# Kernel optimization log

Hardware: AMD Instinct MI355X
Metric: run time of the kernel (lower is better)

The kernel has to match this reference:

```python
import jax, jax.numpy as jnp
import numpy as np

EPS = 1e-12  # torch F.normalize eps


def _normalize(x):
    n = jnp.sqrt(jnp.sum(x * x, axis=1, keepdims=True))
    return x / jnp.maximum(n, EPS)


def _exp_sim(a, b, temp):
    # exp(a @ b.T / temp); returns (diag [B], row_sum [B,1])
    m = jnp.exp(jnp.matmul(a, b.T) / temp)
    return jnp.diagonal(m), jnp.sum(m, axis=1, keepdims=True)


def reference(x):
    temp = 0.1
    bsz = x.shape[0] // 3
    xn = _normalize(x)
    xe, ye, ze = xn[:bsz], xn[bsz:2 * bsz], xn[2 * bsz:]

    d_xx, s_xx = _exp_sim(xe, xe, temp)
    d_yy, s_yy = _exp_sim(ye, ye, temp)
    d_xy, s_xy = _exp_sim(xe, ye, temp)
    d_ax, s_ax = _exp_sim(xe, ze, temp)
    d_ay, s_ay = _exp_sim(ye, ze, temp)
    d_zx, s_zx = _exp_sim(ze, xe, temp)
    d_zy, s_zy = _exp_sim(ze, ye, temp)

    # NOTE: diag terms are [B], row-sums are [B,1] -> denominator broadcasts to
    # [B,B], matching the original torch broadcasting exactly.
    denom_mutual = (s_xy - d_xy) + (s_xx - d_xx) + (s_yy - d_yy)  # [B,B]
    loss_mutual = jnp.mean(-2.0 * jnp.log(d_xy / denom_mutual))

    def aux(d, s):
        return jnp.mean(-jnp.log(d / (s - d)))  # d/[B,B] -> [B,B]

    loss = (loss_mutual + aux(d_ax, s_ax) + aux(d_ay, s_ay)
            + aux(d_zx, s_zx) + aux(d_zy, s_zy))
    return loss


def setup_inputs() -> dict:
    key = jax.random.key(0)
    x = jax.random.normal(key, (12288, 128), dtype=jnp.float32)
    return {"x": x}
```

## Files before the change

### kernel.cpp

```cpp
#include <hip/hip_runtime.h>
#include <hip/hip_bf16.h>


typedef __attribute__((ext_vector_type(8))) short short8;
typedef __attribute__((ext_vector_type(4))) float floatx4;

#define D   128
#define BSZ 4096
#define GPM 256
#define GRID_EXPSIM (5 * 16 * 16)

__global__ __launch_bounds__(256) void normalize_kernel(
    const float* __restrict__ x, __hip_bfloat162* __restrict__ xnf2,
    float* __restrict__ out, int rows) {
  int tid = threadIdx.x;
  if (blockIdx.x == 0 && tid == 0) out[0] = 0.0f;

  int row  = blockIdx.x * 4 + (tid >> 6);
  int lane = tid & 63;
  if (row >= rows) return;
  const float2* xr = (const float2*)(x + (size_t)row * D);
  float2 v = xr[lane];
  float s = v.x * v.x + v.y * v.y;
#pragma unroll
  for (int off = 1; off < 64; off <<= 1) s += __shfl_xor(s, off, 64);
  float scale = 3.7982825470322528f / fmaxf(sqrtf(s), 1e-12f);
  __hip_bfloat162 h;
  h.x = __float2bfloat16(v.x * scale);
  h.y = __float2bfloat16(v.y * scale);
  int g    = row >> 4;
  int kk   = lane >> 4;
  int quad = (lane >> 2) & 3;
  int jj   = lane & 3;
  xnf2[g * 1024 + kk * 256 + (quad * 16 + (row & 15)) * 4 + jj] = h;
}

template <bool COL, bool DIAG>
__device__ __forceinline__ void epilogue(
    const floatx4 (&acc)[4][4], float (&rs)[4][4], float (&cs)[4],
    int rowg0, int colg0, int quad, int lm, float* __restrict__ diag_ptr) {
#pragma unroll
  for (int mi = 0; mi < 4; mi++) {
#pragma unroll
    for (int r = 0; r < 4; r++) {
      int rowg = rowg0 + mi * 16 + quad * 4 + r;
      float part = 0.f;
#pragma unroll
      for (int ni = 0; ni < 4; ni++) {
        float e = __builtin_amdgcn_exp2f(acc[mi][ni][r]);
        part += e;
        if (COL) cs[ni] += e;
        if (DIAG) {
          if (colg0 + ni * 16 + lm == rowg) diag_ptr[rowg] = e;
        }
      }
      rs[mi][r] += part;
    }
  }
}

__global__ __launch_bounds__(256) void expsim_kernel(
    const short8* __restrict__ xnf8,
    float* __restrict__ srow,
    float* __restrict__ scol,
    float* __restrict__ diag) {
  __shared__ float csLDS[4 * 256];

  int tid = threadIdx.x;
  int bx  = blockIdx.x;
  int task = bx >> 8;
  int rem  = bx & 255;
  int rb   = rem >> 4;
  int cb   = rem & 15;

  const int aoff_t[5] = {0, 1, 0, 0, 1};
  const int boff_t[5] = {0, 1, 1, 2, 2};
  bool col_en = (task >= 3);

  int w    = tid >> 6;
  int lane = tid & 63;
  int quad = lane >> 4;
  int lm   = lane & 15;
  int rowg0 = rb * 256 + w * 64;

  bool dgblk = (rb == cb);

  float* diag_ptr = diag + task * BSZ;

  int gA = aoff_t[task] * GPM + rb * 16 + w * 4;
  short8 afrag[4][4];
#pragma unroll
  for (int mi = 0; mi < 4; mi++)
#pragma unroll
    for (int kk = 0; kk < 4; kk++)
      afrag[mi][kk] = xnf8[(size_t)(gA + mi) * 256 + kk * 64 + lane];

  float rs[4][4];
#pragma unroll
  for (int mi = 0; mi < 4; mi++)
#pragma unroll
    for (int r = 0; r < 4; r++) rs[mi][r] = 0.0f;

  const floatx4 z4 = {0.f, 0.f, 0.f, 0.f};
  const short8* bbase = xnf8 + (size_t)(boff_t[task] * GPM + cb * 16) * 256 + lane;

#pragma unroll 1
  for (int t = 0; t < 4; t++) {
    int colg0 = cb * 256 + t * 64;

    short8 bf[16];
#pragma unroll
    for (int i = 0; i < 16; i++)
      bf[i] = bbase[(size_t)(t * 4 + (i & 3)) * 256 + (i >> 2) * 64];

    floatx4 acc[4][4];
#pragma unroll
    for (int kk = 0; kk < 4; kk++)
#pragma unroll
      for (int mi = 0; mi < 4; mi++)
#pragma unroll
        for (int ni = 0; ni < 4; ni++)
          acc[mi][ni] = __builtin_amdgcn_mfma_f32_16x16x32_bf16(
              afrag[mi][kk], bf[kk * 4 + ni], (kk == 0) ? z4 : acc[mi][ni],
              0, 0, 0);

    float cs[4] = {0.f, 0.f, 0.f, 0.f};
    bool dg = dgblk && (t == w);
    if (col_en) {
      if (dg) epilogue<true, true>(acc, rs, cs, rowg0, colg0, quad, lm, diag_ptr);
      else    epilogue<true, false>(acc, rs, cs, rowg0, colg0, quad, lm, diag_ptr);
#pragma unroll
      for (int ni = 0; ni < 4; ni++) {
        float v = cs[ni];
        v += __shfl_xor(v, 16, 64);
        v += __shfl_xor(v, 32, 64);
        if (quad == 0) csLDS[w * 256 + t * 64 + ni * 16 + lm] = v;
      }
    } else {
      if (dg) epilogue<false, true>(acc, rs, cs, rowg0, colg0, quad, lm, diag_ptr);
      else    epilogue<false, false>(acc, rs, cs, rowg0, colg0, quad, lm, diag_ptr);
    }
  }

  float* srow_ptr = srow + ((size_t)(task * 16 + cb)) * BSZ;
#pragma unroll
  for (int mi = 0; mi < 4; mi++) {
#pragma unroll
    for (int r = 0; r < 4; r++) {
      float v = rs[mi][r];
      v += __shfl_xor(v, 1, 64);
      v += __shfl_xor(v, 2, 64);
      v += __shfl_xor(v, 4, 64);
      v += __shfl_xor(v, 8, 64);
      if (lm == 0) srow_ptr[rowg0 + mi * 16 + quad * 4 + r] = v;
    }
  }

  if (col_en) {
    __syncthreads();
    float* scol_ptr = scol + ((size_t)((task - 3) * 16 + rb)) * BSZ + cb * 256;
    scol_ptr[tid] = csLDS[tid] + csLDS[256 + tid] + csLDS[512 + tid] + csLDS[768 + tid];
  }
}

__global__ __launch_bounds__(256) void reduce_kernel(
    const float* __restrict__ srow, const float* __restrict__ scol,
    const float* __restrict__ diag, float* __restrict__ out) {
  int tid = threadIdx.x;
  int i   = blockIdx.x * 256 + tid;

  float s[5];
#pragma unroll
  for (int t = 0; t < 5; t++) {
    float a = 0.f;
#pragma unroll
    for (int js = 0; js < 16; js++) a += srow[(size_t)(t * 16 + js) * BSZ + i];
    s[t] = a;
  }
  float s_zx = 0.f, s_zy = 0.f;
#pragma unroll 8
  for (int ib = 0; ib < 16; ib++) {
    s_zx += scol[(size_t)ib * BSZ + i];
    s_zy += scol[(size_t)(16 + ib) * BSZ + i];
  }
  float d_xx = diag[0 * BSZ + i], d_yy = diag[1 * BSZ + i];
  float d_xy = diag[2 * BSZ + i], d_ax = diag[3 * BSZ + i];
  float d_ay = diag[4 * BSZ + i];

  float denom = (s[2] - d_xy) + (s[0] - d_xx) + (s[1] - d_yy);
  float tloc = -2.0f * __logf(d_xy / denom);
  tloc -= __logf(d_ax / (s[3] - d_ax));
  tloc -= __logf(d_ay / (s[4] - d_ay));
  tloc -= __logf(d_ax / (s_zx - d_ax));
  tloc -= __logf(d_ay / (s_zy - d_ay));

  __shared__ float red[256];
  red[tid] = tloc;
  __syncthreads();
  for (int st = 128; st > 0; st >>= 1) {
    if (tid < st) red[tid] += red[tid + st];
    __syncthreads();
  }
  if (tid == 0) atomicAdd(out, red[0] / (float)BSZ);
}

extern "C" void kernel_launch(void* const* d_in, const int* in_sizes, int n_in,
                              void* d_out, int out_size, void* d_ws, size_t ws_size,
                              hipStream_t stream) {
  const float* x = (const float*)d_in[0];
  int rows = in_sizes[0] / D;

  char*  ws       = (char*)d_ws;
  short* xnf      = (short*)ws;
  size_t xn_bytes = (size_t)rows * D * sizeof(short);
  float* srow     = (float*)(ws + xn_bytes);
  float* scol     = srow + 5 * 16 * BSZ;
  float* diag     = scol + 2 * 16 * BSZ;

  normalize_kernel<<<rows / 4, 256, 0, stream>>>(
      x, (__hip_bfloat162*)xnf, (float*)d_out, rows);
  expsim_kernel<<<GRID_EXPSIM, 256, 0, stream>>>(
      (const short8*)xnf, srow, scol, diag);
  reduce_kernel<<<16, 256, 0, stream>>>(srow, scol, diag, (float*)d_out);
}
```

Baseline: 97.21 us.

## Software-pipeline B fragment loads with double-buffered 16-column sub-tiles

Restructures the expsim inner loop from 4 iterations of 64 columns into 16 fully unrolled sub-steps of 16 columns. B fragments are double-buffered, so the next sub-tile's global loads are issued before the current MFMAs and exp epilogue, overlapping load latency with compute. This also cuts live accumulator registers from 16 floatx4 to 4, which may improve occupancy, but full unrolling enlarges the code and the column-sum shuffles now run per 16-column sub-tile.

```diff
diff --git a/kernel.cpp b/kernel.cpp
--- a/kernel.cpp
+++ b/kernel.cpp
@@ -36,25 +36,20 @@
 }
 
 template <bool COL, bool DIAG>
-__device__ __forceinline__ void epilogue(
-    const floatx4 (&acc)[4][4], float (&rs)[4][4], float (&cs)[4],
+__device__ __forceinline__ void epi_sub(
+    const floatx4 (&acc)[4], float (&rs)[4][4], float& cs,
     int rowg0, int colg0, int quad, int lm, float* __restrict__ diag_ptr) {
 #pragma unroll
   for (int mi = 0; mi < 4; mi++) {
 #pragma unroll
     for (int r = 0; r < 4; r++) {
-      int rowg = rowg0 + mi * 16 + quad * 4 + r;
-      float part = 0.f;
-#pragma unroll
-      for (int ni = 0; ni < 4; ni++) {
-        float e = __builtin_amdgcn_exp2f(acc[mi][ni][r]);
-        part += e;
-        if (COL) cs[ni] += e;
-        if (DIAG) {
-          if (colg0 + ni * 16 + lm == rowg) diag_ptr[rowg] = e;
-        }
+      float e = __builtin_amdgcn_exp2f(acc[mi][r]);
+      rs[mi][r] += e;
+      if (COL) cs += e;
+      if (DIAG) {
+        int rowg = rowg0 + mi * 16 + quad * 4 + r;
+        if (colg0 + lm == rowg) diag_ptr[rowg] = e;
       }
-      rs[mi][r] += part;
     }
   }
 }
@@ -104,41 +99,45 @@
   const floatx4 z4 = {0.f, 0.f, 0.f, 0.f};
   const short8* bbase = xnf8 + (size_t)(boff_t[task] * GPM + cb * 16) * 256 + lane;
 
-#pragma unroll 1
-  for (int t = 0; t < 4; t++) {
-    int colg0 = cb * 256 + t * 64;
-
-    short8 bf[16];
-#pragma unroll
-    for (int i = 0; i < 16; i++)
-      bf[i] = bbase[(size_t)(t * 4 + (i & 3)) * 256 + (i >> 2) * 64];
-
-    floatx4 acc[4][4];
+  short8 bf0[4], bf1[4];
+#pragma unroll
+  for (int kk = 0; kk < 4; kk++) bf0[kk] = bbase[(size_t)kk * 64];
+
+#pragma unroll
+  for (int s = 0; s < 16; s++) {
+    if (s < 15) {
+      if ((s & 1) == 0) {
+#pragma unroll
+        for (int kk = 0; kk < 4; kk++)
+          bf1[kk] = bbase[(size_t)(s + 1) * 256 + kk * 64];
+      } else {
+#pragma unroll
+        for (int kk = 0; kk < 4; kk++)
+          bf0[kk] = bbase[(size_t)(s + 1) * 256 + kk * 64];
+      }
+    }
+    const short8(&bf)[4] = (s & 1) ? bf1 : bf0;
+
+    floatx4 acc[4];
 #pragma unroll
     for (int kk = 0; kk < 4; kk++)
 #pragma unroll
       for (int mi = 0; mi < 4; mi++)
-#pragma unroll
-        for (int ni = 0; ni < 4; ni++)
-          acc[mi][ni] = __builtin_amdgcn_mfma_f32_16x16x32_bf16(
-              afrag[mi][kk], bf[kk * 4 + ni], (kk == 0) ? z4 : acc[mi][ni],
-              0, 0, 0);
-
-    float cs[4] = {0.f, 0.f, 0.f, 0.f};
-    bool dg = dgblk && (t == w);
+        acc[mi] = __builtin_amdgcn_mfma_f32_16x16x32_bf16(
+            afrag[mi][kk], bf[kk], (kk == 0) ? z4 : acc[mi], 0, 0, 0);
+
+    int colg0 = cb * 256 + s * 16;
+    float cs = 0.f;
+    bool dg = dgblk && ((s >> 2) == w);
     if (col_en) {
-      if (dg) epilogue<true, true>(acc, rs, cs, rowg0, colg0, quad, lm, diag_ptr);
-      else    epilogue<true, false>(acc, rs, cs, rowg0, colg0, quad, lm, diag_ptr);
-#pragma unroll
-      for (int ni = 0; ni < 4; ni++) {
-        float v = cs[ni];
-        v += __shfl_xor(v, 16, 64);
-        v += __shfl_xor(v, 32, 64);
-        if (quad == 0) csLDS[w * 256 + t * 64 + ni * 16 + lm] = v;
-      }
+      if (dg) epi_sub<true, true>(acc, rs, cs, rowg0, colg0, quad, lm, diag_ptr);
+      else    epi_sub<true, false>(acc, rs, cs, rowg0, colg0, quad, lm, diag_ptr);
+      cs += __shfl_xor(cs, 16, 64);
+      cs += __shfl_xor(cs, 32, 64);
+      if (quad == 0) csLDS[w * 256 + s * 16 + lm] = cs;
     } else {
-      if (dg) epilogue<false, true>(acc, rs, cs, rowg0, colg0, quad, lm, diag_ptr);
-      else    epilogue<false, false>(acc, rs, cs, rowg0, colg0, quad, lm, diag_ptr);
+      if (dg) epi_sub<false, true>(acc, rs, cs, rowg0, colg0, quad, lm, diag_ptr);
+      else    epi_sub<false, false>(acc, rs, cs, rowg0, colg0, quad, lm, diag_ptr);
     }
   }
 
```

Result: slower. 113.6 us (+16.8%).
